# Kernel tuning notes

Measured on AMD Instinct MI355X. Metric: run time of the kernel, lower is better.

The kernel has to match this reference:

```python
import jax, jax.numpy as jnp
import numpy as np

N_NODES = 50000
N_EDGES = 1600000
D_FEAT = 32


def setup_inputs() -> dict:
    key = jax.random.key(0)
    k1, k2, k3, k4 = jax.random.split(key, 4)
    node_feat = jax.random.normal(k1, (N_NODES, D_FEAT), dtype=jnp.float32)
    edge_feat = jax.random.normal(k2, (N_EDGES, D_FEAT), dtype=jnp.float32)
    eps = jnp.zeros((1,), dtype=jnp.float32)  # learnable eps, init 0
    src = jax.random.randint(k3, (N_EDGES,), 0, N_NODES, dtype=jnp.int64)
    dst = jax.random.randint(k4, (N_EDGES,), 0, N_NODES, dtype=jnp.int64)
    return {"node_feat": node_feat, "edge_feat": edge_feat, "eps": eps,
            "src": src, "dst": dst}


def reference(node_feat, edge_feat, eps, src, dst):
    # message: relu(h_src + h_edge) per edge  [E, D]
    m = jax.nn.relu(node_feat[src] + edge_feat)
    # sum-aggregate messages into destination nodes  [N, D]
    neigh = jax.ops.segment_sum(m, dst, num_segments=node_feat.shape[0])
    # eps-scaled residual
    return (1.0 + eps[0]) * node_feat + neigh
```

## Files before the change

kernel.cpp:

```cpp
#include <hip/hip_runtime.h>

#define N_NODES 50000
#define N_EDGES 1600000
#define D_FEAT 32
#define SCAN_BLOCK 1024
#define N_SCAN_BLOCKS ((N_NODES + SCAN_BLOCK - 1) / SCAN_BLOCK)

#define WS_CNT   0
#define WS_EXCL  (N_NODES)
#define WS_BSUM  (2 * N_NODES)
#define WS_BSUMX (2 * N_NODES + 64)
#define WS_RANK  (2 * N_NODES + 128)
#define WS_PAIR  (2 * N_NODES + 128 + N_EDGES)

typedef float f4 __attribute__((ext_vector_type(4)));


__global__ void hist_rank(const int* __restrict__ dst,
                          int* __restrict__ cnt,
                          int* __restrict__ rank) {
    int q = blockIdx.x * blockDim.x + threadIdx.x;
    const int NQ = N_EDGES / 4;
    if (q >= NQ) return;
    int4 d4 = ((const int4*)dst)[q];
    int4 r4;
    r4.x = atomicAdd(&cnt[d4.x], 1);
    r4.y = atomicAdd(&cnt[d4.y], 1);
    r4.z = atomicAdd(&cnt[d4.z], 1);
    r4.w = atomicAdd(&cnt[d4.w], 1);
    ((int4*)rank)[q] = r4;
}

__global__ void scan_blocks(const int* __restrict__ cnt,
                            int* __restrict__ excl,
                            int* __restrict__ bsum) {
    __shared__ int lds[SCAN_BLOCK];
    int tid = threadIdx.x;
    int i = blockIdx.x * SCAN_BLOCK + tid;
    int v = (i < N_NODES) ? cnt[i] : 0;
    int sum = v;
    lds[tid] = v;
    __syncthreads();
    for (int ofs = 1; ofs < SCAN_BLOCK; ofs <<= 1) {
        int t = (tid >= ofs) ? lds[tid - ofs] : 0;
        __syncthreads();
        sum += t;
        lds[tid] = sum;
        __syncthreads();
    }
    if (i < N_NODES) excl[i] = sum - v;
    if (tid == SCAN_BLOCK - 1) bsum[blockIdx.x] = lds[SCAN_BLOCK - 1];
}

__global__ void scan_bsums(const int* __restrict__ bsum, int* __restrict__ bsumx) {
    int lane = threadIdx.x;
    int orig = (lane < N_SCAN_BLOCKS) ? bsum[lane] : 0;
    int v = orig;
    for (int o = 1; o < 64; o <<= 1) {
        int t = __shfl_up(v, o);
        if (lane >= o) v += t;
    }
    if (lane < N_SCAN_BLOCKS) bsumx[lane] = v - orig;
}

__global__ void scatter_pairs(const int* __restrict__ src,
                              const int* __restrict__ dst,
                              const int* __restrict__ excl,
                              const int* __restrict__ bsumx,
                              const int* __restrict__ rank,
                              int2* __restrict__ pair) {
    int q = blockIdx.x * blockDim.x + threadIdx.x;
    const int NQ = N_EDGES / 4;
    if (q >= NQ) return;
    int4 d4 = ((const int4*)dst)[q];
    int4 s4 = ((const int4*)src)[q];
    int4 r4 = ((const int4*)rank)[q];
    int e0 = q * 4;
    pair[excl[d4.x] + bsumx[d4.x >> 10] + r4.x] = make_int2(e0,     s4.x);
    pair[excl[d4.y] + bsumx[d4.y >> 10] + r4.y] = make_int2(e0 + 1, s4.y);
    pair[excl[d4.z] + bsumx[d4.z >> 10] + r4.z] = make_int2(e0 + 2, s4.z);
    pair[excl[d4.w] + bsumx[d4.w >> 10] + r4.w] = make_int2(e0 + 3, s4.w);
}

__global__ void reduce_gather(const float* __restrict__ node_feat,
                              const float* __restrict__ edge_feat,
                              const float* __restrict__ eps,
                              const int* __restrict__ excl,
                              const int* __restrict__ bsumx,
                              const int* __restrict__ cnt,
                              const int2* __restrict__ pair,
                              float* __restrict__ out) {
    int t = blockIdx.x * blockDim.x + threadIdx.x;
    int n = t >> 3;
    int g = t & 7;
    if (n >= N_NODES) return;

    int start = excl[n] + bsumx[n >> 10];
    int c = cnt[n];
    int gbase = (threadIdx.x & 63) & ~7;

    const f4* efp = (const f4*)edge_feat;
    const f4* nfp = (const f4*)node_feat;

    f4 acc = (f4)(0.f);
    int i0 = 0;
    for (; i0 + 8 <= c; i0 += 8) {
        int2 p = pair[start + i0 + g];
#pragma unroll
        for (int j = 0; j < 8; ++j) {
            int e = __shfl(p.x, gbase + j);
            int s = __shfl(p.y, gbase + j);
            f4 ef = __builtin_nontemporal_load(&efp[(size_t)e * 8 + g]);
            f4 nf = nfp[(size_t)s * 8 + g];
            acc.x += fmaxf(nf.x + ef.x, 0.f);
            acc.y += fmaxf(nf.y + ef.y, 0.f);
            acc.z += fmaxf(nf.z + ef.z, 0.f);
            acc.w += fmaxf(nf.w + ef.w, 0.f);
        }
    }
    int rem = c - i0;
    if (rem > 0) {
        int2 p = (g < rem) ? pair[start + i0 + g] : make_int2(0, 0);
        for (int j = 0; j < rem; ++j) {
            int e = __shfl(p.x, gbase + j);
            int s = __shfl(p.y, gbase + j);
            f4 ef = __builtin_nontemporal_load(&efp[(size_t)e * 8 + g]);
            f4 nf = nfp[(size_t)s * 8 + g];
            acc.x += fmaxf(nf.x + ef.x, 0.f);
            acc.y += fmaxf(nf.y + ef.y, 0.f);
            acc.z += fmaxf(nf.z + ef.z, 0.f);
            acc.w += fmaxf(nf.w + ef.w, 0.f);
        }
    }

    float scale = 1.0f + eps[0];
    f4 h = nfp[(size_t)n * 8 + g];
    f4 o;
    o.x = scale * h.x + acc.x;
    o.y = scale * h.y + acc.y;
    o.z = scale * h.z + acc.z;
    o.w = scale * h.w + acc.w;
    ((f4*)out)[(size_t)n * 8 + g] = o;
}


__global__ void fb_init_out(const float* __restrict__ node_feat,
                            const float* __restrict__ eps,
                            float* __restrict__ out) {
    int i = blockIdx.x * blockDim.x + threadIdx.x;
    const int n4 = N_NODES * D_FEAT / 4;
    float scale = 1.0f + eps[0];
    if (i < n4) {
        float4 v = ((const float4*)node_feat)[i];
        v.x *= scale; v.y *= scale; v.z *= scale; v.w *= scale;
        ((float4*)out)[i] = v;
    }
}

__global__ void fb_scatter(const float* __restrict__ node_feat,
                           const float* __restrict__ edge_feat,
                           const int* __restrict__ src,
                           const int* __restrict__ dst,
                           float* __restrict__ out) {
    int t = blockIdx.x * blockDim.x + threadIdx.x;
    int e = t >> 3;
    int g = t & 7;
    if (e >= N_EDGES) return;
    int s = src[e];
    int d = dst[e];
    float4 nf = ((const float4*)node_feat)[s * 8 + g];
    float4 ef = ((const float4*)edge_feat)[(size_t)e * 8 + g];
    float* op = out + (size_t)d * D_FEAT + g * 4;
    unsafeAtomicAdd(op + 0, fmaxf(nf.x + ef.x, 0.f));
    unsafeAtomicAdd(op + 1, fmaxf(nf.y + ef.y, 0.f));
    unsafeAtomicAdd(op + 2, fmaxf(nf.z + ef.z, 0.f));
    unsafeAtomicAdd(op + 3, fmaxf(nf.w + ef.w, 0.f));
}

extern "C" void kernel_launch(void* const* d_in, const int* in_sizes, int n_in,
                              void* d_out, int out_size, void* d_ws, size_t ws_size,
                              hipStream_t stream) {
    const float* node_feat = (const float*)d_in[0];
    const float* edge_feat = (const float*)d_in[1];
    const float* eps       = (const float*)d_in[2];
    const int*   src       = (const int*)d_in[3];
    const int*   dst       = (const int*)d_in[4];
    float* out = (float*)d_out;

    const int B = 256;
    const size_t need = ((size_t)WS_PAIR + 2ull * N_EDGES) * sizeof(int);

    if (ws_size < need) {
        int n4 = N_NODES * D_FEAT / 4;
        fb_init_out<<<(n4 + B - 1) / B, B, 0, stream>>>(node_feat, eps, out);
        long long total = (long long)N_EDGES * 8;
        fb_scatter<<<(int)((total + B - 1) / B), B, 0, stream>>>(
            node_feat, edge_feat, src, dst, out);
        return;
    }

    int* ws = (int*)d_ws;
    int*  cnt   = ws + WS_CNT;
    int*  excl  = ws + WS_EXCL;
    int*  bsum  = ws + WS_BSUM;
    int*  bsumx = ws + WS_BSUMX;
    int*  rank  = ws + WS_RANK;
    int2* pair  = (int2*)(ws + WS_PAIR);

    hipMemsetAsync(cnt, 0, N_NODES * sizeof(int), stream);

    int nq = N_EDGES / 4;
    hist_rank<<<(nq + B - 1) / B, B, 0, stream>>>(dst, cnt, rank);
    scan_blocks<<<N_SCAN_BLOCKS, SCAN_BLOCK, 0, stream>>>(cnt, excl, bsum);
    scan_bsums<<<1, 64, 0, stream>>>(bsum, bsumx);

    scatter_pairs<<<(nq + B - 1) / B, B, 0, stream>>>(
        src, dst, excl, bsumx, rank, pair);

    long long ntotal = (long long)N_NODES * 8;
    reduce_gather<<<(int)((ntotal + B - 1) / B), B, 0, stream>>>(
        node_feat, edge_feat, eps, excl, bsumx, cnt, pair, out);
}
```

Measured before the change: 427.7 us.

## Switch CSR gather to edge-balanced fixed-size chunks with boundary atomics

Replaces the per-node gather, where each 8-lane group processed one node's variable-length edge list, with fixed 64-edge chunks over the sorted pair array. Each chunk binary-searches its starting node in a new finalized offsets array and flushes partial sums with float atomics at segment boundaries. Output is pre-initialised with the scaled residual by a separate kernel. This aims to remove load imbalance and tail-loop overhead. The cost is extra kernels, a binary search per chunk, atomics on output rows, and nondeterministic summation order.

Result: no change. 427.1 us (-0.1%).

```diff
diff --git a/kernel.cpp b/kernel.cpp
--- a/kernel.cpp
+++ b/kernel.cpp
@@ -5,13 +5,16 @@
 #define D_FEAT 32
 #define SCAN_BLOCK 1024
 #define N_SCAN_BLOCKS ((N_NODES + SCAN_BLOCK - 1) / SCAN_BLOCK)
+#define CHUNK 64
+#define NCHUNK (N_EDGES / CHUNK)
 
 #define WS_CNT   0
 #define WS_EXCL  (N_NODES)
-#define WS_BSUM  (2 * N_NODES)
-#define WS_BSUMX (2 * N_NODES + 64)
-#define WS_RANK  (2 * N_NODES + 128)
-#define WS_PAIR  (2 * N_NODES + 128 + N_EDGES)
+#define WS_OFF   (2 * N_NODES)
+#define WS_BSUM  (3 * N_NODES + 64)
+#define WS_BSUMX (3 * N_NODES + 128)
+#define WS_RANK  (3 * N_NODES + 192)
+#define WS_PAIR  (3 * N_NODES + 192 + N_EDGES)
 
 typedef float f4 __attribute__((ext_vector_type(4)));
 
@@ -63,10 +66,17 @@
     if (lane < N_SCAN_BLOCKS) bsumx[lane] = v - orig;
 }
 
+__global__ void finalize_off(const int* __restrict__ excl,
+                             const int* __restrict__ bsumx,
+                             int* __restrict__ off) {
+    int i = blockIdx.x * SCAN_BLOCK + threadIdx.x;
+    if (i < N_NODES) off[i] = excl[i] + bsumx[blockIdx.x];
+    else if (i == N_NODES) off[i] = N_EDGES;
+}
+
 __global__ void scatter_pairs(const int* __restrict__ src,
                               const int* __restrict__ dst,
-                              const int* __restrict__ excl,
-                              const int* __restrict__ bsumx,
+                              const int* __restrict__ off,
                               const int* __restrict__ rank,
                               int2* __restrict__ pair) {
     int q = blockIdx.x * blockDim.x + threadIdx.x;
@@ -76,38 +86,64 @@
     int4 s4 = ((const int4*)src)[q];
     int4 r4 = ((const int4*)rank)[q];
     int e0 = q * 4;
-    pair[excl[d4.x] + bsumx[d4.x >> 10] + r4.x] = make_int2(e0,     s4.x);
-    pair[excl[d4.y] + bsumx[d4.y >> 10] + r4.y] = make_int2(e0 + 1, s4.y);
-    pair[excl[d4.z] + bsumx[d4.z >> 10] + r4.z] = make_int2(e0 + 2, s4.z);
-    pair[excl[d4.w] + bsumx[d4.w >> 10] + r4.w] = make_int2(e0 + 3, s4.w);
-}
-
-__global__ void reduce_gather(const float* __restrict__ node_feat,
+    pair[off[d4.x] + r4.x] = make_int2(e0,     s4.x);
+    pair[off[d4.y] + r4.y] = make_int2(e0 + 1, s4.y);
+    pair[off[d4.z] + r4.z] = make_int2(e0 + 2, s4.z);
+    pair[off[d4.w] + r4.w] = make_int2(e0 + 3, s4.w);
+}
+
+__global__ void init_out(const float* __restrict__ node_feat,
+                         const float* __restrict__ eps,
+                         float* __restrict__ out) {
+    int i = blockIdx.x * blockDim.x + threadIdx.x;
+    const int n4 = N_NODES * D_FEAT / 4;
+    float scale = 1.0f + eps[0];
+    if (i < n4) {
+        float4 v = ((const float4*)node_feat)[i];
+        v.x *= scale; v.y *= scale; v.z *= scale; v.w *= scale;
+        ((float4*)out)[i] = v;
+    }
+}
+
+__global__ void reduce_chunks(const float* __restrict__ node_feat,
                               const float* __restrict__ edge_feat,
-                              const float* __restrict__ eps,
-                              const int* __restrict__ excl,
-                              const int* __restrict__ bsumx,
-                              const int* __restrict__ cnt,
+                              const int* __restrict__ off,
                               const int2* __restrict__ pair,
                               float* __restrict__ out) {
     int t = blockIdx.x * blockDim.x + threadIdx.x;
-    int n = t >> 3;
+    int grp = t >> 3;
     int g = t & 7;
-    if (n >= N_NODES) return;
-
-    int start = excl[n] + bsumx[n >> 10];
-    int c = cnt[n];
+    if (grp >= NCHUNK) return;
+    int p0 = grp * CHUNK;
     int gbase = (threadIdx.x & 63) & ~7;
+
+    int lo = 0, hi = N_NODES - 1;
+    while (lo < hi) {
+        int mid = (lo + hi + 1) >> 1;
+        if (off[mid] <= p0) lo = mid; else hi = mid - 1;
+    }
+    int n = lo;
+    int segEnd = off[n + 1];
 
     const f4* efp = (const f4*)edge_feat;
     const f4* nfp = (const f4*)node_feat;
 
     f4 acc = (f4)(0.f);
-    int i0 = 0;
-    for (; i0 + 8 <= c; i0 += 8) {
-        int2 p = pair[start + i0 + g];
+    for (int k = 0; k < CHUNK; k += 8) {
+        int2 p = pair[p0 + k + g];
 #pragma unroll
         for (int j = 0; j < 8; ++j) {
+            int pos = p0 + k + j;
+            while (pos == segEnd) {
+                float* op = out + (size_t)n * D_FEAT + g * 4;
+                unsafeAtomicAdd(op + 0, acc.x);
+                unsafeAtomicAdd(op + 1, acc.y);
+                unsafeAtomicAdd(op + 2, acc.z);
+                unsafeAtomicAdd(op + 3, acc.w);
+                acc = (f4)(0.f);
+                ++n;
+                segEnd = off[n + 1];
+            }
             int e = __shfl(p.x, gbase + j);
             int s = __shfl(p.y, gbase + j);
             f4 ef = __builtin_nontemporal_load(&efp[(size_t)e * 8 + g]);
@@ -118,44 +154,13 @@
             acc.w += fmaxf(nf.w + ef.w, 0.f);
         }
     }
-    int rem = c - i0;
-    if (rem > 0) {
-        int2 p = (g < rem) ? pair[start + i0 + g] : make_int2(0, 0);
-        for (int j = 0; j < rem; ++j) {
-            int e = __shfl(p.x, gbase + j);
-            int s = __shfl(p.y, gbase + j);
-            f4 ef = __builtin_nontemporal_load(&efp[(size_t)e * 8 + g]);
-            f4 nf = nfp[(size_t)s * 8 + g];
-            acc.x += fmaxf(nf.x + ef.x, 0.f);
-            acc.y += fmaxf(nf.y + ef.y, 0.f);
-            acc.z += fmaxf(nf.z + ef.z, 0.f);
-            acc.w += fmaxf(nf.w + ef.w, 0.f);
-        }
-    }
-
-    float scale = 1.0f + eps[0];
-    f4 h = nfp[(size_t)n * 8 + g];
-    f4 o;
-    o.x = scale * h.x + acc.x;
-    o.y = scale * h.y + acc.y;
-    o.z = scale * h.z + acc.z;
-    o.w = scale * h.w + acc.w;
-    ((f4*)out)[(size_t)n * 8 + g] = o;
-}
-
-
-__global__ void fb_init_out(const float* __restrict__ node_feat,
-                            const float* __restrict__ eps,
-                            float* __restrict__ out) {
-    int i = blockIdx.x * blockDim.x + threadIdx.x;
-    const int n4 = N_NODES * D_FEAT / 4;
-    float scale = 1.0f + eps[0];
-    if (i < n4) {
-        float4 v = ((const float4*)node_feat)[i];
-        v.x *= scale; v.y *= scale; v.z *= scale; v.w *= scale;
-        ((float4*)out)[i] = v;
-    }
-}
+    float* op = out + (size_t)n * D_FEAT + g * 4;
+    unsafeAtomicAdd(op + 0, acc.x);
+    unsafeAtomicAdd(op + 1, acc.y);
+    unsafeAtomicAdd(op + 2, acc.z);
+    unsafeAtomicAdd(op + 3, acc.w);
+}
+
 
 __global__ void fb_scatter(const float* __restrict__ node_feat,
                            const float* __restrict__ edge_feat,
@@ -192,7 +197,7 @@
 
     if (ws_size < need) {
         int n4 = N_NODES * D_FEAT / 4;
-        fb_init_out<<<(n4 + B - 1) / B, B, 0, stream>>>(node_feat, eps, out);
+        init_out<<<(n4 + B - 1) / B, B, 0, stream>>>(node_feat, eps, out);
         long long total = (long long)N_EDGES * 8;
         fb_scatter<<<(int)((total + B - 1) / B), B, 0, stream>>>(
             node_feat, edge_feat, src, dst, out);
@@ -202,6 +207,7 @@
     int* ws = (int*)d_ws;
     int*  cnt   = ws + WS_CNT;
     int*  excl  = ws + WS_EXCL;
+    int*  off   = ws + WS_OFF;
     int*  bsum  = ws + WS_BSUM;
     int*  bsumx = ws + WS_BSUMX;
     int*  rank  = ws + WS_RANK;
@@ -213,11 +219,14 @@
     hist_rank<<<(nq + B - 1) / B, B, 0, stream>>>(dst, cnt, rank);
     scan_blocks<<<N_SCAN_BLOCKS, SCAN_BLOCK, 0, stream>>>(cnt, excl, bsum);
     scan_bsums<<<1, 64, 0, stream>>>(bsum, bsumx);
-
-    scatter_pairs<<<(nq + B - 1) / B, B, 0, stream>>>(
-        src, dst, excl, bsumx, rank, pair);
-
-    long long ntotal = (long long)N_NODES * 8;
-    reduce_gather<<<(int)((ntotal + B - 1) / B), B, 0, stream>>>(
-        node_feat, edge_feat, eps, excl, bsumx, cnt, pair, out);
-}
+    finalize_off<<<N_SCAN_BLOCKS, SCAN_BLOCK, 0, stream>>>(excl, bsumx, off);
+
+    scatter_pairs<<<(nq + B - 1) / B, B, 0, stream>>>(src, dst, off, rank, pair);
+
+    int n4 = N_NODES * D_FEAT / 4;
+    init_out<<<(n4 + B - 1) / B, B, 0, stream>>>(node_feat, eps, out);
+
+    long long rtotal = (long long)NCHUNK * 8;
+    reduce_chunks<<<(int)((rtotal + B - 1) / B), B, 0, stream>>>(
+        node_feat, edge_feat, off, pair, out);
+}
```
